# Kernel optimization log

Hardware: AMD Instinct MI355X
Metric: run time of the kernel (lower is better)

Reference implementation:

```python
import jax, jax.numpy as jnp
import numpy as np

BATCH, SEQ_LEN, INPUT_DIM = 64, 8192, 1
RESERVOIR_DIM = 80
DELAY_TAPS = [1, 4, 24, 96, 168]
MAX_DELAY = max(DELAY_TAPS)
SPECTRAL_RADIUS = 0.9
INPUT_SCALING = 0.5
LEAK_RATE = 0.3
SEED = 42
# buf[:, MAX_DELAY - tau] holds h_{t - tau} (zeros if t - tau < 0)
TAP_IDX = np.array([MAX_DELAY - tau for tau in DELAY_TAPS])


def setup_inputs() -> dict:
    key = jax.random.key(0)
    x = jax.random.normal(key, (BATCH, SEQ_LEN, INPUT_DIM), dtype=jnp.float32)
    rng = np.random.default_rng(SEED)
    W_in = rng.uniform(-INPUT_SCALING, INPUT_SCALING, size=(RESERVOIR_DIM, INPUT_DIM))
    W_fb_list = []
    for tau in DELAY_TAPS:
        W_k = rng.standard_normal((RESERVOIR_DIM, RESERVOIR_DIM))
        max_eig = np.max(np.abs(np.linalg.eigvals(W_k)))
        if max_eig > 0:
            W_k = W_k * (SPECTRAL_RADIUS / len(DELAY_TAPS)) / max_eig
        W_fb_list.append(W_k)
    W_fb = np.stack(W_fb_list, axis=0)  # (K, R, R)
    bias = rng.uniform(-0.1, 0.1, size=RESERVOIR_DIM)
    return {
        "x": x,
        "W_in": jnp.asarray(W_in, dtype=jnp.float32),
        "W_fb": jnp.asarray(W_fb, dtype=jnp.float32),
        "bias": jnp.asarray(bias, dtype=jnp.float32),
    }


def reference(x, W_in, W_fb, bias):
    B, S, _ = x.shape
    R = W_in.shape[0]
    # Precompute input drive for all timesteps: (S, B, R) for scan over time.
    drive = jnp.einsum("bsi,ri->sbr", x, W_in)
    h0 = jnp.zeros((B, R), dtype=x.dtype)
    buf0 = jnp.zeros((B, MAX_DELAY, R), dtype=x.dtype)  # rolling history

    def step(carry, drive_t):
        h, buf = carry
        delayed = buf[:, TAP_IDX, :]  # (B, K, R): h_{t-tau} for each tap
        # feedback = sum_k delayed_k @ W_fb_k.T
        feedback = jnp.einsum("bkj,kij->bi", delayed, W_fb)
        h_new = (1.0 - LEAK_RATE) * h + LEAK_RATE * jnp.tanh(drive_t + feedback + bias)
        buf = jnp.concatenate([buf[:, 1:], h_new[:, None, :]], axis=1)
        return (h_new, buf), h_new

    (_, _), states = jax.lax.scan(step, (h0, buf0), drive)
    return jnp.transpose(states, (1, 0, 2))  # (B, S, R)
```

## Files before the change

kernel.cpp:

```cpp
#include <hip/hip_runtime.h>

#define BATCH 64
#define SEQ 8192
#define RDIM 80
#define RING 169
#define NCHUNK (SEQ / 2)

typedef float v2f __attribute__((ext_vector_type(2)));

__device__ __forceinline__ float fast_tanh(float z) {
    float e = __expf(2.0f * z);
    return 1.0f - 2.0f / (e + 1.0f);
}

template <int CTRL>
__device__ __forceinline__ float dpp_xor_add(float v) {
    int o = __builtin_amdgcn_mov_dpp(__float_as_int(v), CTRL, 0xF, 0xF, true);
    return v + __int_as_float(o);
}

__global__ __attribute__((amdgpu_flat_work_group_size(256, 256),
                          amdgpu_waves_per_eu(1, 1)))
void reservoir_kernel(const float* __restrict__ x,
                      const float* __restrict__ W_in,
                      const float* __restrict__ W_fb,
                      const float* __restrict__ bias,
                      float* __restrict__ out) {
    __shared__ __align__(16) float ring[RING * RDIM];
    __shared__ __align__(16) float h_hist[4 * RDIM];

    const int b    = blockIdx.x;
    const int t    = threadIdx.x;
    const int wid  = t >> 6;
    const int lane = t & 63;

    for (int i = t; i < RING * RDIM; i += 256) ring[i] = 0.0f;
    for (int i = t; i < 4 * RDIM; i += 256) h_hist[i] = 0.0f;

    const float* xb   = x + (size_t)b * SEQ;
    float*       outb = out + (size_t)b * (size_t)SEQ * RDIM;

    v2f wr2[80];

    int q = 0, sub = 0, rowA = 0, rowB = 0;
    float hA = 0.f, hB = 0.f, winA = 0.f, winB = 0.f, bA = 0.f, bB = 0.f;
    v2f hh2[10];
    int tap_tau = 0, qq = 0, half = 0;
    bool tap_valid = false, tap_lo = false;
    float x0 = 0.f, x1 = 0.f;

    if (wid == 0) {
        q = lane >> 2; sub = lane & 3;
        rowA = 5 * q + sub;
        rowB = 5 * q + 4;
        #pragma unroll
        for (int r = 0; r < 5; ++r) {
            const float* src = W_fb + (size_t)(5 * q + r) * RDIM + 20 * sub;
            #pragma unroll
            for (int j4 = 0; j4 < 5; ++j4) {
                float4 v = ((const float4*)src)[j4];
                wr2[r * 10 + 2 * j4 + 0] = (v2f){v.x, v.y};
                wr2[r * 10 + 2 * j4 + 1] = (v2f){v.z, v.w};
            }
        }
        winA = W_in[rowA]; bA = bias[rowA];
        winB = W_in[rowB]; bB = bias[rowB];
        #pragma unroll
        for (int j2 = 0; j2 < 10; ++j2) hh2[j2] = (v2f){0.f, 0.f};
        x0 = xb[0]; x1 = xb[1];
    } else {
        int g = (wid - 1) * 64 + lane;
        tap_valid = (g < 160);
        int gg = tap_valid ? g : 159;
        int k = gg / 40, rem = gg % 40;
        qq = rem >> 1; half = rem & 1;
        tap_lo = (half == 0);
        const int taus[4] = {4, 24, 96, 168};
        tap_tau = taus[k];
        #pragma unroll
        for (int r = 0; r < 4; ++r) {
            const float* src = W_fb + (size_t)(k + 1) * RDIM * RDIM
                                    + (size_t)(4 * qq + r) * RDIM + 40 * half;
            #pragma unroll
            for (int j4 = 0; j4 < 10; ++j4) {
                float4 v = ((const float4*)src)[j4];
                wr2[r * 20 + 2 * j4 + 0] = (v2f){v.x, v.y};
                wr2[r * 20 + 2 * j4 + 1] = (v2f){v.z, v.w};
            }
        }
    }

    __syncthreads();

    for (int c = 0; c < NCHUNK; ++c) {
        if (wid == 0) {
            const int s0  = 2 * c;
            const int sl0 = s0 % RING, sl1 = (s0 + 1) % RING;
            float rgA0 = ring[sl0 * RDIM + rowA];
            float rgA1 = ring[sl1 * RDIM + rowA];
            float rgB0 = 0.f, rgB1 = 0.f;
            if (sub == 0) { rgB0 = ring[sl0 * RDIM + rowB]; rgB1 = ring[sl1 * RDIM + rowB]; }
            ring[sl0 * RDIM + rowA] = 0.f; ring[sl1 * RDIM + rowA] = 0.f;
            if (sub == 0) { ring[sl0 * RDIM + rowB] = 0.f; ring[sl1 * RDIM + rowB] = 0.f; }
            float xn0 = x0, xn1 = x1;
            if (s0 + 2 < SEQ) { float2 xn = *(const float2*)(xb + s0 + 2); xn0 = xn.x; xn1 = xn.y; }

            #pragma unroll
            for (int st = 0; st < 2; ++st) {
                const int s     = s0 + st;
                const float xs  = st ? x1   : x0;
                const float rgA = st ? rgA1 : rgA0;
                const float rgB = st ? rgB1 : rgB0;
                v2f dd2[5];
                #pragma unroll
                for (int r = 0; r < 5; ++r) dd2[r] = (v2f){0.f, 0.f};
                #pragma unroll
                for (int r = 0; r < 5; ++r)
                    #pragma unroll
                    for (int j2 = 0; j2 < 10; ++j2)
                        dd2[r] = __builtin_elementwise_fma(wr2[r * 10 + j2], hh2[j2], dd2[r]);
                float dd[5];
                #pragma unroll
                for (int r = 0; r < 5; ++r) dd[r] = dd2[r].x + dd2[r].y;
                #pragma unroll
                for (int r = 0; r < 5; ++r) {
                    dd[r] = dpp_xor_add<0xB1>(dd[r]);
                    dd[r] = dpp_xor_add<0x4E>(dd[r]);
                }
                float dA = (sub == 0) ? dd[0] : (sub == 1) ? dd[1] : (sub == 2) ? dd[2] : dd[3];
                float zA = dA + rgA + bA + xs * winA;
                hA = 0.7f * hA + 0.3f * fast_tanh(zA);
                if (sub == 0) {
                    float zB = dd[4] + rgB + bB + xs * winB;
                    hB = 0.7f * hB + 0.3f * fast_tanh(zB);
                }
                h_hist[(s & 3) * RDIM + rowA] = hA;
                if (sub == 0) h_hist[(s & 3) * RDIM + rowB] = hB;
                {
                    const float4* hp = (const float4*)(h_hist + (s & 3) * RDIM + 20 * sub);
                    #pragma unroll
                    for (int j4 = 0; j4 < 5; ++j4) {
                        float4 v = hp[j4];
                        hh2[2 * j4 + 0] = (v2f){v.x, v.y};
                        hh2[2 * j4 + 1] = (v2f){v.z, v.w};
                    }
                }
                outb[(size_t)s * RDIM + rowA] = hA;
                if (sub == 0) outb[(size_t)s * RDIM + rowB] = hB;
            }
            x0 = xn0; x1 = xn1;
        } else if (c > 0) {
            const int sp0 = 2 * (c - 1);
            #pragma unroll
            for (int st = 0; st < 2; ++st) {
                const int sp = sp0 + st;
                const float* hp = h_hist + (sp & 3) * RDIM + 40 * half;
                v2f ha2[20];
                #pragma unroll
                for (int j4 = 0; j4 < 10; ++j4) {
                    float4 v = ((const float4*)hp)[j4];
                    ha2[2 * j4 + 0] = (v2f){v.x, v.y};
                    ha2[2 * j4 + 1] = (v2f){v.z, v.w};
                }
                v2f dA2[4];
                #pragma unroll
                for (int r = 0; r < 4; ++r) dA2[r] = (v2f){0.f, 0.f};
                #pragma unroll
                for (int r = 0; r < 4; ++r)
                    #pragma unroll
                    for (int j2 = 0; j2 < 20; ++j2)
                        dA2[r] = __builtin_elementwise_fma(wr2[r * 20 + j2], ha2[j2], dA2[r]);
                float dA[4];
                #pragma unroll
                for (int r = 0; r < 4; ++r) dA[r] = dA2[r].x + dA2[r].y;
                #pragma unroll
                for (int r = 0; r < 4; ++r)
                    dA[r] = dpp_xor_add<0xB1>(dA[r]);
                if (tap_valid && tap_lo) {
                    const int sl = (sp + tap_tau) % RING;
                    float4* pA = (float4*)(ring + sl * RDIM + 4 * qq);
                    float4 vA = *pA;
                    vA.x += dA[0]; vA.y += dA[1]; vA.z += dA[2]; vA.w += dA[3];
                    *pA = vA;
                }
            }
        }
        asm volatile("s_waitcnt lgkmcnt(0)" ::: "memory");
        __builtin_amdgcn_s_barrier();
    }
}

extern "C" void kernel_launch(void* const* d_in, const int* in_sizes, int n_in,
                              void* d_out, int out_size, void* d_ws, size_t ws_size,
                              hipStream_t stream) {
    const float* x    = (const float*)d_in[0];
    const float* W_in = (const float*)d_in[1];
    const float* W_fb = (const float*)d_in[2];
    const float* bias = (const float*)d_in[3];
    float* out        = (float*)d_out;

    reservoir_kernel<<<BATCH, 256, 0, stream>>>(x, W_in, W_fb, bias, out);
}
```

Before: 3.450 ms.

## Process two batch rows per block to interleave independent recurrences

Each block now handles two batch elements, each with its own shared-memory ring and history buffer, and interleaves the two independent recurrence chains inside the same wave so their latencies overlap. The grid is halved to 32 blocks, so fewer CUs are used, but per-step latency such as DPP reductions, LDS round-trips and barriers is amortized over two sequences. The risk is that the serial critical path per step grows, so the dependent chain per step roughly doubles while the number of steps stays the same.

```diff
diff --git a/kernel.cpp b/kernel.cpp
--- a/kernel.cpp
+++ b/kernel.cpp
@@ -26,28 +26,32 @@
                       const float* __restrict__ W_fb,
                       const float* __restrict__ bias,
                       float* __restrict__ out) {
-    __shared__ __align__(16) float ring[RING * RDIM];
-    __shared__ __align__(16) float h_hist[4 * RDIM];
-
-    const int b    = blockIdx.x;
+    __shared__ __align__(16) float ring[2 * RING * RDIM];
+    __shared__ __align__(16) float h_hist[2 * 4 * RDIM];
+
     const int t    = threadIdx.x;
     const int wid  = t >> 6;
     const int lane = t & 63;
-
-    for (int i = t; i < RING * RDIM; i += 256) ring[i] = 0.0f;
-    for (int i = t; i < 4 * RDIM; i += 256) h_hist[i] = 0.0f;
-
-    const float* xb   = x + (size_t)b * SEQ;
-    float*       outb = out + (size_t)b * (size_t)SEQ * RDIM;
+    const int b0   = blockIdx.x * 2;
+
+    for (int i = t; i < 2 * RING * RDIM; i += 256) ring[i] = 0.0f;
+    for (int i = t; i < 2 * 4 * RDIM; i += 256) h_hist[i] = 0.0f;
+
+    float* ringp[2] = { ring, ring + RING * RDIM };
+    float* hhp[2]   = { h_hist, h_hist + 4 * RDIM };
+    const float* xb[2] = { x + (size_t)b0 * SEQ, x + (size_t)(b0 + 1) * SEQ };
+    float* ob[2] = { out + (size_t)b0 * (size_t)SEQ * RDIM,
+                     out + (size_t)(b0 + 1) * (size_t)SEQ * RDIM };
 
     v2f wr2[80];
 
     int q = 0, sub = 0, rowA = 0, rowB = 0;
-    float hA = 0.f, hB = 0.f, winA = 0.f, winB = 0.f, bA = 0.f, bB = 0.f;
-    v2f hh2[10];
+    float winA = 0.f, winB = 0.f, bA = 0.f, bB = 0.f;
+    float hA[2] = {0.f, 0.f}, hB[2] = {0.f, 0.f};
+    v2f hh2[2][10];
     int tap_tau = 0, qq = 0, half = 0;
     bool tap_valid = false, tap_lo = false;
-    float x0 = 0.f, x1 = 0.f;
+    float x0[2] = {0.f, 0.f}, x1[2] = {0.f, 0.f};
 
     if (wid == 0) {
         q = lane >> 2; sub = lane & 3;
@@ -66,8 +70,11 @@
         winA = W_in[rowA]; bA = bias[rowA];
         winB = W_in[rowB]; bB = bias[rowB];
         #pragma unroll
-        for (int j2 = 0; j2 < 10; ++j2) hh2[j2] = (v2f){0.f, 0.f};
-        x0 = xb[0]; x1 = xb[1];
+        for (int pb = 0; pb < 2; ++pb)
+            #pragma unroll
+            for (int j2 = 0; j2 < 10; ++j2) hh2[pb][j2] = (v2f){0.f, 0.f};
+        x0[0] = xb[0][0]; x1[0] = xb[0][1];
+        x0[1] = xb[1][0]; x1[1] = xb[1][1];
     } else {
         int g = (wid - 1) * 64 + lane;
         tap_valid = (g < 160);
@@ -96,92 +103,114 @@
         if (wid == 0) {
             const int s0  = 2 * c;
             const int sl0 = s0 % RING, sl1 = (s0 + 1) % RING;
-            float rgA0 = ring[sl0 * RDIM + rowA];
-            float rgA1 = ring[sl1 * RDIM + rowA];
-            float rgB0 = 0.f, rgB1 = 0.f;
-            if (sub == 0) { rgB0 = ring[sl0 * RDIM + rowB]; rgB1 = ring[sl1 * RDIM + rowB]; }
-            ring[sl0 * RDIM + rowA] = 0.f; ring[sl1 * RDIM + rowA] = 0.f;
-            if (sub == 0) { ring[sl0 * RDIM + rowB] = 0.f; ring[sl1 * RDIM + rowB] = 0.f; }
-            float xn0 = x0, xn1 = x1;
-            if (s0 + 2 < SEQ) { float2 xn = *(const float2*)(xb + s0 + 2); xn0 = xn.x; xn1 = xn.y; }
+            float rgA0[2], rgA1[2], rgB0[2] = {0.f, 0.f}, rgB1[2] = {0.f, 0.f};
+            #pragma unroll
+            for (int pb = 0; pb < 2; ++pb) {
+                rgA0[pb] = ringp[pb][sl0 * RDIM + rowA];
+                rgA1[pb] = ringp[pb][sl1 * RDIM + rowA];
+                if (sub == 0) {
+                    rgB0[pb] = ringp[pb][sl0 * RDIM + rowB];
+                    rgB1[pb] = ringp[pb][sl1 * RDIM + rowB];
+                }
+                ringp[pb][sl0 * RDIM + rowA] = 0.f; ringp[pb][sl1 * RDIM + rowA] = 0.f;
+                if (sub == 0) { ringp[pb][sl0 * RDIM + rowB] = 0.f; ringp[pb][sl1 * RDIM + rowB] = 0.f; }
+            }
+            float xn0[2] = { x0[0], x0[1] }, xn1[2] = { x1[0], x1[1] };
+            if (s0 + 2 < SEQ) {
+                #pragma unroll
+                for (int pb = 0; pb < 2; ++pb) {
+                    float2 xn = *(const float2*)(xb[pb] + s0 + 2);
+                    xn0[pb] = xn.x; xn1[pb] = xn.y;
+                }
+            }
 
             #pragma unroll
             for (int st = 0; st < 2; ++st) {
-                const int s     = s0 + st;
-                const float xs  = st ? x1   : x0;
-                const float rgA = st ? rgA1 : rgA0;
-                const float rgB = st ? rgB1 : rgB0;
-                v2f dd2[5];
-                #pragma unroll
-                for (int r = 0; r < 5; ++r) dd2[r] = (v2f){0.f, 0.f};
-                #pragma unroll
-                for (int r = 0; r < 5; ++r)
-                    #pragma unroll
-                    for (int j2 = 0; j2 < 10; ++j2)
-                        dd2[r] = __builtin_elementwise_fma(wr2[r * 10 + j2], hh2[j2], dd2[r]);
-                float dd[5];
-                #pragma unroll
-                for (int r = 0; r < 5; ++r) dd[r] = dd2[r].x + dd2[r].y;
-                #pragma unroll
-                for (int r = 0; r < 5; ++r) {
-                    dd[r] = dpp_xor_add<0xB1>(dd[r]);
-                    dd[r] = dpp_xor_add<0x4E>(dd[r]);
-                }
-                float dA = (sub == 0) ? dd[0] : (sub == 1) ? dd[1] : (sub == 2) ? dd[2] : dd[3];
-                float zA = dA + rgA + bA + xs * winA;
-                hA = 0.7f * hA + 0.3f * fast_tanh(zA);
-                if (sub == 0) {
-                    float zB = dd[4] + rgB + bB + xs * winB;
-                    hB = 0.7f * hB + 0.3f * fast_tanh(zB);
-                }
-                h_hist[(s & 3) * RDIM + rowA] = hA;
-                if (sub == 0) h_hist[(s & 3) * RDIM + rowB] = hB;
-                {
-                    const float4* hp = (const float4*)(h_hist + (s & 3) * RDIM + 20 * sub);
-                    #pragma unroll
-                    for (int j4 = 0; j4 < 5; ++j4) {
-                        float4 v = hp[j4];
-                        hh2[2 * j4 + 0] = (v2f){v.x, v.y};
-                        hh2[2 * j4 + 1] = (v2f){v.z, v.w};
-                    }
-                }
-                outb[(size_t)s * RDIM + rowA] = hA;
-                if (sub == 0) outb[(size_t)s * RDIM + rowB] = hB;
-            }
-            x0 = xn0; x1 = xn1;
+                const int s = s0 + st;
+                #pragma unroll
+                for (int pb = 0; pb < 2; ++pb) {
+                    const float xs  = st ? x1[pb]   : x0[pb];
+                    const float rgA = st ? rgA1[pb] : rgA0[pb];
+                    const float rgB = st ? rgB1[pb] : rgB0[pb];
+                    v2f dd2[5];
+                    #pragma unroll
+                    for (int r = 0; r < 5; ++r) dd2[r] = (v2f){0.f, 0.f};
+                    #pragma unroll
+                    for (int r = 0; r < 5; ++r)
+                        #pragma unroll
+                        for (int j2 = 0; j2 < 10; ++j2)
+                            dd2[r] = __builtin_elementwise_fma(wr2[r * 10 + j2], hh2[pb][j2], dd2[r]);
+                    float dd[5];
+                    #pragma unroll
+                    for (int r = 0; r < 5; ++r) dd[r] = dd2[r].x + dd2[r].y;
+                    #pragma unroll
+                    for (int r = 0; r < 5; ++r) {
+                        dd[r] = dpp_xor_add<0xB1>(dd[r]);
+                        dd[r] = dpp_xor_add<0x4E>(dd[r]);
+                    }
+                    float dA = (sub == 0) ? dd[0] : (sub == 1) ? dd[1] : (sub == 2) ? dd[2] : dd[3];
+                    float zA = dA + rgA + bA + xs * winA;
+                    hA[pb] = 0.7f * hA[pb] + 0.3f * fast_tanh(zA);
+                    if (sub == 0) {
+                        float zB = dd[4] + rgB + bB + xs * winB;
+                        hB[pb] = 0.7f * hB[pb] + 0.3f * fast_tanh(zB);
+                    }
+                    hhp[pb][(s & 3) * RDIM + rowA] = hA[pb];
+                    if (sub == 0) hhp[pb][(s & 3) * RDIM + rowB] = hB[pb];
+                    {
+                        const float4* hp = (const float4*)(hhp[pb] + (s & 3) * RDIM + 20 * sub);
+                        #pragma unroll
+                        for (int j4 = 0; j4 < 5; ++j4) {
+                            float4 v = hp[j4];
+                            hh2[pb][2 * j4 + 0] = (v2f){v.x, v.y};
+                            hh2[pb][2 * j4 + 1] = (v2f){v.z, v.w};
+                        }
+                    }
+                    ob[pb][(size_t)s * RDIM + rowA] = hA[pb];
+                    if (sub == 0) ob[pb][(size_t)s * RDIM + rowB] = hB[pb];
+                }
+            }
+            x0[0] = xn0[0]; x0[1] = xn0[1];
+            x1[0] = xn1[0]; x1[1] = xn1[1];
         } else if (c > 0) {
             const int sp0 = 2 * (c - 1);
             #pragma unroll
             for (int st = 0; st < 2; ++st) {
                 const int sp = sp0 + st;
-                const float* hp = h_hist + (sp & 3) * RDIM + 40 * half;
-                v2f ha2[20];
-                #pragma unroll
-                for (int j4 = 0; j4 < 10; ++j4) {
-                    float4 v = ((const float4*)hp)[j4];
-                    ha2[2 * j4 + 0] = (v2f){v.x, v.y};
-                    ha2[2 * j4 + 1] = (v2f){v.z, v.w};
-                }
-                v2f dA2[4];
-                #pragma unroll
-                for (int r = 0; r < 4; ++r) dA2[r] = (v2f){0.f, 0.f};
-                #pragma unroll
-                for (int r = 0; r < 4; ++r)
-                    #pragma unroll
-                    for (int j2 = 0; j2 < 20; ++j2)
-                        dA2[r] = __builtin_elementwise_fma(wr2[r * 20 + j2], ha2[j2], dA2[r]);
-                float dA[4];
-                #pragma unroll
-                for (int r = 0; r < 4; ++r) dA[r] = dA2[r].x + dA2[r].y;
-                #pragma unroll
-                for (int r = 0; r < 4; ++r)
-                    dA[r] = dpp_xor_add<0xB1>(dA[r]);
-                if (tap_valid && tap_lo) {
-                    const int sl = (sp + tap_tau) % RING;
-                    float4* pA = (float4*)(ring + sl * RDIM + 4 * qq);
-                    float4 vA = *pA;
-                    vA.x += dA[0]; vA.y += dA[1]; vA.z += dA[2]; vA.w += dA[3];
-                    *pA = vA;
+                const int sl = (sp + tap_tau) % RING;
+                v2f ha2[2][20];
+                #pragma unroll
+                for (int pb = 0; pb < 2; ++pb) {
+                    const float* hp = hhp[pb] + (sp & 3) * RDIM + 40 * half;
+                    #pragma unroll
+                    for (int j4 = 0; j4 < 10; ++j4) {
+                        float4 v = ((const float4*)hp)[j4];
+                        ha2[pb][2 * j4 + 0] = (v2f){v.x, v.y};
+                        ha2[pb][2 * j4 + 1] = (v2f){v.z, v.w};
+                    }
+                }
+                #pragma unroll
+                for (int pb = 0; pb < 2; ++pb) {
+                    v2f dA2[4];
+                    #pragma unroll
+                    for (int r = 0; r < 4; ++r) dA2[r] = (v2f){0.f, 0.f};
+                    #pragma unroll
+                    for (int r = 0; r < 4; ++r)
+                        #pragma unroll
+                        for (int j2 = 0; j2 < 20; ++j2)
+                            dA2[r] = __builtin_elementwise_fma(wr2[r * 20 + j2], ha2[pb][j2], dA2[r]);
+                    float dA[4];
+                    #pragma unroll
+                    for (int r = 0; r < 4; ++r) dA[r] = dA2[r].x + dA2[r].y;
+                    #pragma unroll
+                    for (int r = 0; r < 4; ++r)
+                        dA[r] = dpp_xor_add<0xB1>(dA[r]);
+                    if (tap_valid && tap_lo) {
+                        float4* pA = (float4*)(ringp[pb] + sl * RDIM + 4 * qq);
+                        float4 vA = *pA;
+                        vA.x += dA[0]; vA.y += dA[1]; vA.z += dA[2]; vA.w += dA[3];
+                        *pA = vA;
+                    }
                 }
             }
         }
@@ -199,5 +228,5 @@
     const float* bias = (const float*)d_in[3];
     float* out        = (float*)d_out;
 
-    reservoir_kernel<<<BATCH, 256, 0, stream>>>(x, W_in, W_fb, bias, out);
-}
+    reservoir_kernel<<<BATCH / 2, 256, 0, stream>>>(x, W_in, W_fb, bias, out);
+}
```

After: 7.041 ms. 2.04x slower.

## Process 8 steps per barrier and move tau-4 tap into the recurrent wave

Applied to the files above, without the earlier changes.

Each barrier now covers 8 timesteps instead of 2, so the block synchronises a quarter as often. The tau=1 and tau=4 feedback terms are both computed inside wave 0 from a 4-deep register history, which lets the delayed taps (24, 96, 168) run one chunk behind, one wave per tap. The ring buffer is resized to 176 slots so it can be indexed by chunk-aligned byte offsets without a modulo. In exchange, wave 0 does twice the FMAs per step on its critical path and needs more registers.

```diff
diff --git a/kernel.cpp b/kernel.cpp
--- a/kernel.cpp
+++ b/kernel.cpp
@@ -3,8 +3,12 @@
 #define BATCH 64
 #define SEQ 8192
 #define RDIM 80
-#define RING 169
-#define NCHUNK (SEQ / 2)
+#define CSTEP 8
+#define NCHUNK (SEQ / CSTEP)
+#define RSLOTS 176
+#define SLOT_B (RDIM * 4)
+#define RING_B (RSLOTS * SLOT_B)
+#define CHUNK_B (CSTEP * SLOT_B)
 
 typedef float v2f __attribute__((ext_vector_type(2)));
 
@@ -26,99 +30,112 @@
                       const float* __restrict__ W_fb,
                       const float* __restrict__ bias,
                       float* __restrict__ out) {
-    __shared__ __align__(16) float ring[RING * RDIM];
-    __shared__ __align__(16) float h_hist[4 * RDIM];
+    __shared__ __align__(16) float ring[RSLOTS * RDIM];
+    __shared__ __align__(16) float h_hist[2 * CSTEP * RDIM];
 
     const int b    = blockIdx.x;
     const int t    = threadIdx.x;
     const int wid  = t >> 6;
     const int lane = t & 63;
 
-    for (int i = t; i < RING * RDIM; i += 256) ring[i] = 0.0f;
-    for (int i = t; i < 4 * RDIM; i += 256) h_hist[i] = 0.0f;
+    for (int i = t; i < RSLOTS * RDIM; i += 256) ring[i] = 0.0f;
+    for (int i = t; i < 2 * CSTEP * RDIM; i += 256) h_hist[i] = 0.0f;
 
     const float* xb   = x + (size_t)b * SEQ;
     float*       outb = out + (size_t)b * (size_t)SEQ * RDIM;
 
-    v2f wr2[80];
-
-    int q = 0, sub = 0, rowA = 0, rowB = 0;
-    float hA = 0.f, hB = 0.f, winA = 0.f, winB = 0.f, bA = 0.f, bB = 0.f;
-    v2f hh2[10];
-    int tap_tau = 0, qq = 0, half = 0;
-    bool tap_valid = false, tap_lo = false;
-    float x0 = 0.f, x1 = 0.f;
-
-    if (wid == 0) {
-        q = lane >> 2; sub = lane & 3;
-        rowA = 5 * q + sub;
-        rowB = 5 * q + 4;
+    const int q = lane >> 2, sub = lane & 3;
+    const int rowA = 5 * q + sub;
+    const int rowB = 5 * q + 4;
+
+    v2f wm[50];
+    {
+        const int km = (wid == 0) ? 0 : (wid + 1);
         #pragma unroll
         for (int r = 0; r < 5; ++r) {
-            const float* src = W_fb + (size_t)(5 * q + r) * RDIM + 20 * sub;
+            const float* src = W_fb + (size_t)km * RDIM * RDIM
+                                    + (size_t)(5 * q + r) * RDIM + 20 * sub;
             #pragma unroll
             for (int j4 = 0; j4 < 5; ++j4) {
                 float4 v = ((const float4*)src)[j4];
-                wr2[r * 10 + 2 * j4 + 0] = (v2f){v.x, v.y};
-                wr2[r * 10 + 2 * j4 + 1] = (v2f){v.z, v.w};
+                wm[r * 10 + 2 * j4 + 0] = (v2f){v.x, v.y};
+                wm[r * 10 + 2 * j4 + 1] = (v2f){v.z, v.w};
+            }
+        }
+    }
+
+    v2f w4[50];
+    float4 hist[4][5];
+    float winA = 0.f, winB = 0.f, bA = 0.f, bB = 0.f, hA = 0.f, hB = 0.f;
+    float4 xc0 = {0,0,0,0}, xc1 = {0,0,0,0};
+    int tap_base = 0;
+    if (wid == 0) {
+        #pragma unroll
+        for (int r = 0; r < 5; ++r) {
+            const float* src = W_fb + (size_t)RDIM * RDIM
+                                    + (size_t)(5 * q + r) * RDIM + 20 * sub;
+            #pragma unroll
+            for (int j4 = 0; j4 < 5; ++j4) {
+                float4 v = ((const float4*)src)[j4];
+                w4[r * 10 + 2 * j4 + 0] = (v2f){v.x, v.y};
+                w4[r * 10 + 2 * j4 + 1] = (v2f){v.z, v.w};
             }
         }
         winA = W_in[rowA]; bA = bias[rowA];
         winB = W_in[rowB]; bB = bias[rowB];
         #pragma unroll
-        for (int j2 = 0; j2 < 10; ++j2) hh2[j2] = (v2f){0.f, 0.f};
-        x0 = xb[0]; x1 = xb[1];
+        for (int i = 0; i < 4; ++i)
+            #pragma unroll
+            for (int j = 0; j < 5; ++j) hist[i][j] = (float4){0.f, 0.f, 0.f, 0.f};
+        xc0 = ((const float4*)xb)[0];
+        xc1 = ((const float4*)xb)[1];
     } else {
-        int g = (wid - 1) * 64 + lane;
-        tap_valid = (g < 160);
-        int gg = tap_valid ? g : 159;
-        int k = gg / 40, rem = gg % 40;
-        qq = rem >> 1; half = rem & 1;
-        tap_lo = (half == 0);
-        const int taus[4] = {4, 24, 96, 168};
-        tap_tau = taus[k];
-        #pragma unroll
-        for (int r = 0; r < 4; ++r) {
-            const float* src = W_fb + (size_t)(k + 1) * RDIM * RDIM
-                                    + (size_t)(4 * qq + r) * RDIM + 40 * half;
-            #pragma unroll
-            for (int j4 = 0; j4 < 10; ++j4) {
-                float4 v = ((const float4*)src)[j4];
-                wr2[r * 20 + 2 * j4 + 0] = (v2f){v.x, v.y};
-                wr2[r * 20 + 2 * j4 + 1] = (v2f){v.z, v.w};
-            }
-        }
+        const int tau = (wid == 1) ? 24 : (wid == 2) ? 96 : 168;
+        tap_base = tau * SLOT_B;
     }
+    int rec_base = 0;
 
     __syncthreads();
 
     for (int c = 0; c < NCHUNK; ++c) {
         if (wid == 0) {
-            const int s0  = 2 * c;
-            const int sl0 = s0 % RING, sl1 = (s0 + 1) % RING;
-            float rgA0 = ring[sl0 * RDIM + rowA];
-            float rgA1 = ring[sl1 * RDIM + rowA];
-            float rgB0 = 0.f, rgB1 = 0.f;
-            if (sub == 0) { rgB0 = ring[sl0 * RDIM + rowB]; rgB1 = ring[sl1 * RDIM + rowB]; }
-            ring[sl0 * RDIM + rowA] = 0.f; ring[sl1 * RDIM + rowA] = 0.f;
-            if (sub == 0) { ring[sl0 * RDIM + rowB] = 0.f; ring[sl1 * RDIM + rowB] = 0.f; }
-            float xn0 = x0, xn1 = x1;
-            if (s0 + 2 < SEQ) { float2 xn = *(const float2*)(xb + s0 + 2); xn0 = xn.x; xn1 = xn.y; }
-
-            #pragma unroll
-            for (int st = 0; st < 2; ++st) {
-                const int s     = s0 + st;
-                const float xs  = st ? x1   : x0;
-                const float rgA = st ? rgA1 : rgA0;
-                const float rgB = st ? rgB1 : rgB0;
+            float rg[8], rgB[8];
+            float* rp = (float*)((char*)ring + rec_base);
+            #pragma unroll
+            for (int st = 0; st < 8; ++st) {
+                rg[st] = rp[st * RDIM + rowA]; rp[st * RDIM + rowA] = 0.f;
+                if (sub == 0) { rgB[st] = rp[st * RDIM + rowB]; rp[st * RDIM + rowB] = 0.f; }
+            }
+            float4 xn0 = xc0, xn1 = xc1;
+            if (c + 1 < NCHUNK) {
+                const float4* xp = (const float4*)(xb + (size_t)(c + 1) * CSTEP);
+                xn0 = xp[0]; xn1 = xp[1];
+            }
+            float* hwp = h_hist + (c & 1) * (CSTEP * RDIM);
+
+            #pragma unroll
+            for (int st = 0; st < 8; ++st) {
+                const int h4 = st & 3;
+                const int h1 = (st + 3) & 3;
                 v2f dd2[5];
                 #pragma unroll
                 for (int r = 0; r < 5; ++r) dd2[r] = (v2f){0.f, 0.f};
                 #pragma unroll
                 for (int r = 0; r < 5; ++r)
                     #pragma unroll
-                    for (int j2 = 0; j2 < 10; ++j2)
-                        dd2[r] = __builtin_elementwise_fma(wr2[r * 10 + j2], hh2[j2], dd2[r]);
+                    for (int j4 = 0; j4 < 5; ++j4) {
+                        const v2f* hv = (const v2f*)&hist[h4][j4];
+                        dd2[r] = __builtin_elementwise_fma(w4[r * 10 + 2 * j4 + 0], hv[0], dd2[r]);
+                        dd2[r] = __builtin_elementwise_fma(w4[r * 10 + 2 * j4 + 1], hv[1], dd2[r]);
+                    }
+                #pragma unroll
+                for (int r = 0; r < 5; ++r)
+                    #pragma unroll
+                    for (int j4 = 0; j4 < 5; ++j4) {
+                        const v2f* hv = (const v2f*)&hist[h1][j4];
+                        dd2[r] = __builtin_elementwise_fma(wm[r * 10 + 2 * j4 + 0], hv[0], dd2[r]);
+                        dd2[r] = __builtin_elementwise_fma(wm[r * 10 + 2 * j4 + 1], hv[1], dd2[r]);
+                    }
                 float dd[5];
                 #pragma unroll
                 for (int r = 0; r < 5; ++r) dd[r] = dd2[r].x + dd2[r].y;
@@ -128,62 +145,60 @@
                     dd[r] = dpp_xor_add<0x4E>(dd[r]);
                 }
                 float dA = (sub == 0) ? dd[0] : (sub == 1) ? dd[1] : (sub == 2) ? dd[2] : dd[3];
-                float zA = dA + rgA + bA + xs * winA;
+                const float xs = (st == 0) ? xc0.x : (st == 1) ? xc0.y : (st == 2) ? xc0.z :
+                                 (st == 3) ? xc0.w : (st == 4) ? xc1.x : (st == 5) ? xc1.y :
+                                 (st == 6) ? xc1.z : xc1.w;
+                float zA = dA + rg[st] + bA + xs * winA;
                 hA = 0.7f * hA + 0.3f * fast_tanh(zA);
                 if (sub == 0) {
-                    float zB = dd[4] + rgB + bB + xs * winB;
+                    float zB = dd[4] + rgB[st] + bB + xs * winB;
                     hB = 0.7f * hB + 0.3f * fast_tanh(zB);
                 }
-                h_hist[(s & 3) * RDIM + rowA] = hA;
-                if (sub == 0) h_hist[(s & 3) * RDIM + rowB] = hB;
+                hwp[st * RDIM + rowA] = hA;
+                if (sub == 0) hwp[st * RDIM + rowB] = hB;
                 {
-                    const float4* hp = (const float4*)(h_hist + (s & 3) * RDIM + 20 * sub);
+                    const float4* hp = (const float4*)(hwp + st * RDIM + 20 * sub);
+                    #pragma unroll
+                    for (int j4 = 0; j4 < 5; ++j4) hist[h4][j4] = hp[j4];
+                }
+                outb[(size_t)(c * CSTEP + st) * RDIM + rowA] = hA;
+                if (sub == 0) outb[(size_t)(c * CSTEP + st) * RDIM + rowB] = hB;
+            }
+            xc0 = xn0; xc1 = xn1;
+            rec_base += CHUNK_B; if (rec_base >= RING_B) rec_base -= RING_B;
+        } else if (c > 0) {
+            const float* hrp = h_hist + ((c - 1) & 1) * (CSTEP * RDIM);
+            float* trp = (float*)((char*)ring + tap_base);
+            #pragma unroll
+            for (int st = 0; st < 8; ++st) {
+                float4 hv4[5];
+                const float4* hp = (const float4*)(hrp + st * RDIM + 20 * sub);
+                #pragma unroll
+                for (int j4 = 0; j4 < 5; ++j4) hv4[j4] = hp[j4];
+                v2f dd2[5];
+                #pragma unroll
+                for (int r = 0; r < 5; ++r) dd2[r] = (v2f){0.f, 0.f};
+                #pragma unroll
+                for (int r = 0; r < 5; ++r)
                     #pragma unroll
                     for (int j4 = 0; j4 < 5; ++j4) {
-                        float4 v = hp[j4];
-                        hh2[2 * j4 + 0] = (v2f){v.x, v.y};
-                        hh2[2 * j4 + 1] = (v2f){v.z, v.w};
+                        const v2f* hv = (const v2f*)&hv4[j4];
+                        dd2[r] = __builtin_elementwise_fma(wm[r * 10 + 2 * j4 + 0], hv[0], dd2[r]);
+                        dd2[r] = __builtin_elementwise_fma(wm[r * 10 + 2 * j4 + 1], hv[1], dd2[r]);
                     }
-                }
-                outb[(size_t)s * RDIM + rowA] = hA;
-                if (sub == 0) outb[(size_t)s * RDIM + rowB] = hB;
-            }
-            x0 = xn0; x1 = xn1;
-        } else if (c > 0) {
-            const int sp0 = 2 * (c - 1);
-            #pragma unroll
-            for (int st = 0; st < 2; ++st) {
-                const int sp = sp0 + st;
-                const float* hp = h_hist + (sp & 3) * RDIM + 40 * half;
-                v2f ha2[20];
-                #pragma unroll
-                for (int j4 = 0; j4 < 10; ++j4) {
-                    float4 v = ((const float4*)hp)[j4];
-                    ha2[2 * j4 + 0] = (v2f){v.x, v.y};
-                    ha2[2 * j4 + 1] = (v2f){v.z, v.w};
-                }
-                v2f dA2[4];
-                #pragma unroll
-                for (int r = 0; r < 4; ++r) dA2[r] = (v2f){0.f, 0.f};
-                #pragma unroll
-                for (int r = 0; r < 4; ++r)
-                    #pragma unroll
-                    for (int j2 = 0; j2 < 20; ++j2)
-                        dA2[r] = __builtin_elementwise_fma(wr2[r * 20 + j2], ha2[j2], dA2[r]);
-                float dA[4];
-                #pragma unroll
-                for (int r = 0; r < 4; ++r) dA[r] = dA2[r].x + dA2[r].y;
-                #pragma unroll
-                for (int r = 0; r < 4; ++r)
-                    dA[r] = dpp_xor_add<0xB1>(dA[r]);
-                if (tap_valid && tap_lo) {
-                    const int sl = (sp + tap_tau) % RING;
-                    float4* pA = (float4*)(ring + sl * RDIM + 4 * qq);
-                    float4 vA = *pA;
-                    vA.x += dA[0]; vA.y += dA[1]; vA.z += dA[2]; vA.w += dA[3];
-                    *pA = vA;
-                }
-            }
+                float dd[5];
+                #pragma unroll
+                for (int r = 0; r < 5; ++r) dd[r] = dd2[r].x + dd2[r].y;
+                #pragma unroll
+                for (int r = 0; r < 5; ++r) {
+                    dd[r] = dpp_xor_add<0xB1>(dd[r]);
+                    dd[r] = dpp_xor_add<0x4E>(dd[r]);
+                }
+                float dA = (sub == 0) ? dd[0] : (sub == 1) ? dd[1] : (sub == 2) ? dd[2] : dd[3];
+                trp[st * RDIM + rowA] += dA;
+                if (sub == 0) trp[st * RDIM + rowB] += dd[4];
+            }
+            tap_base += CHUNK_B; if (tap_base >= RING_B) tap_base -= RING_B;
         }
         asm volatile("s_waitcnt lgkmcnt(0)" ::: "memory");
         __builtin_amdgcn_s_barrier();
```

Result: slower. 4.882 ms (+41.5%).
